# Kernel optimization log

Measured on AMD Instinct MI355X. Metric: run time of the kernel, lower is better.

## Reference

```python
import jax, jax.numpy as jnp
import numpy as np

N, D = 16384, 512
MARGIN = 2.0
EPS = 1e-6  # torch TripletMarginLoss default eps added inside pairwise distance


def setup_inputs() -> dict:
    key = jax.random.key(0)
    k1, k2 = jax.random.split(key)
    inputs = jax.random.normal(k1, (N, D), dtype=jnp.float32)
    positive = jax.random.normal(k2, (N, D), dtype=jnp.float32)
    return {"inputs": inputs, "positive": positive}


def reference(inputs, positive):
    # pairwise squared euclidean distances: ||xi||^2 + ||xj||^2 - 2 xi.xj
    sq = jnp.sum(inputs * inputs, axis=1)                      # [n]
    dist2 = sq[:, None] + sq[None, :] - 2.0 * (inputs @ inputs.T)  # [n,n]
    dist = jnp.sqrt(jnp.clip(dist2, 1e-12))                    # [n,n]
    # original does full argsort per row but only uses index 2 (3rd smallest);
    # top_k on negated distances selects the 3 smallest efficiently.
    _, idx3 = jax.lax.top_k(-dist, 3)                          # [n,3]
    negative = inputs[idx3[:, 2]]                              # [n,d]
    # TripletMarginLoss(margin, p=2): mean(relu(||a-p+eps|| - ||a-n+eps|| + m))
    d_ap = jnp.linalg.norm(inputs - positive + EPS, axis=1)
    d_an = jnp.linalg.norm(inputs - negative + EPS, axis=1)
    loss = jnp.mean(jnp.maximum(d_ap - d_an + MARGIN, 0.0))
    return loss
```

## Files before the change

kernel.cpp:

```cpp
#include <hip/hip_runtime.h>
#include <hip/hip_bf16.h>
#include <hip/hip_fp8.h>
#include <stdint.h>

#define NN 16384
#define DD 512
#define MARGINV 2.0f
#define EPSV 1e-6f

#define BJ 32
#define JGROUPS 8
#define JRANGE (NN / JGROUPS)
#define NTILES (JRANGE / BJ)
#define ROWQ 512
#define TILEB (BJ * ROWQ)
#define SQOFF (2 * TILEB)

#define KEYMASK  0xFFFFC000
#define KEYINITF __builtin_bit_cast(float, 0x7F000000)
#define BIASV 640.0f

typedef __attribute__((ext_vector_type(4))) float f32x4;
typedef __attribute__((ext_vector_type(4))) int   i32x4;
typedef __attribute__((ext_vector_type(8))) int   i32x8;

#define UNIT_SCALE 0x7F

__device__ inline void kins3f(float u, float& m0, float& m1, float& m2) {
  m2 = __builtin_amdgcn_fmed3f(m1, m2, u);
  m1 = __builtin_amdgcn_fmed3f(m0, m1, u);
  m0 = fminf(m0, u);
}

extern "C" __global__ __launch_bounds__(256)
void prep_kernel(const float* __restrict__ x, unsigned char* __restrict__ xq,
                 float* __restrict__ sqb, float* __restrict__ out) {
  if (blockIdx.x == 0 && threadIdx.x == 0) out[0] = 0.0f;
  int row  = blockIdx.x * 4 + (threadIdx.x >> 6);
  int lane = threadIdx.x & 63;
  const float* xr = x + (size_t)row * DD + lane * 8;
  f32x4 a = *(const f32x4*)xr;
  f32x4 b = *(const f32x4*)(xr + 4);
  float s = a[0]*a[0]+a[1]*a[1]+a[2]*a[2]+a[3]*a[3]
          + b[0]*b[0]+b[1]*b[1]+b[2]*b[2]+b[3]*b[3];
  #pragma unroll
  for (int off = 1; off < 64; off <<= 1) s += __shfl_xor(s, off, 64);
  unsigned long long pk = 0;
  #pragma unroll
  for (int t = 0; t < 4; ++t) {
    __hip_fp8_e4m3 qa(a[t]), qb(b[t]);
    pk |= ((unsigned long long)qa.__x) << (8 * t);
    pk |= ((unsigned long long)qb.__x) << (8 * (t + 4));
  }
  *(unsigned long long*)(xq + (size_t)row * ROWQ + lane * 8) = pk;
  if (lane == 0) sqb[row] = s + BIASV;
}

extern "C" __global__ __launch_bounds__(256, 2)
void knn_kernel(const unsigned char* __restrict__ xq, const float* __restrict__ sqb,
                int* __restrict__ pk) {
  __shared__ __align__(16) char lds[2 * TILEB + 8192];
  const int tid  = threadIdx.x;
  const int wave = tid >> 6;
  const int lane = tid & 63;
  const int quad = lane >> 4;
  const int r16  = lane & 15;
  const int bi   = blockIdx.x >> 3;
  const int bj   = blockIdx.x & 7;
  const int ibase = bi * 256 + wave * 64;
  const int jbase = bj * JRANGE;

  #pragma unroll
  for (int p = 0; p < 2; ++p) {
    const float* gs = sqb + jbase + p * 1024 + wave * 256 + lane * 4;
    char* ld = lds + SQOFF + p * 4096 + wave * 1024;
    __builtin_amdgcn_global_load_lds((const __attribute__((address_space(1))) void*)gs,
                                     (__attribute__((address_space(3))) void*)ld,
                                     16, 0, 0);
  }

  i32x8 afr[4][4];
  #pragma unroll
  for (int s = 0; s < 4; ++s) {
    const unsigned char* ar = xq + (size_t)(ibase + s * 16 + r16) * ROWQ + quad * 32;
    #pragma unroll
    for (int c = 0; c < 4; ++c)
      afr[s][c] = *(const i32x8*)(ar + c * 128);
  }

  float m0[16], m1[16], m2[16];
  #pragma unroll
  for (int q = 0; q < 16; ++q) { m0[q] = m1[q] = m2[q] = KEYINITF; }

  auto stage = [&](int jt, int buf) {
    const int jrow0 = jbase + jt * BJ;
    #pragma unroll
    for (int p = 0; p < 4; ++p) {
      const int rr = wave * 8 + p * 2;
      const int lr = rr + (lane >> 5);
      const int u  = (lane & 31) ^ (lr & 7);
      const unsigned char* gsrc = xq + (size_t)(jrow0 + lr) * ROWQ + u * 16;
      char* ldst = lds + buf * TILEB + rr * ROWQ;
      __builtin_amdgcn_global_load_lds((const __attribute__((address_space(1))) void*)gsrc,
                                       (__attribute__((address_space(3))) void*)ldst,
                                       16, 0, 0);
    }
  };

  const int sw = r16 & 7;
  stage(0, 0);
  for (int jt = 0; jt < NTILES; ++jt) {
    __syncthreads();
    if (jt + 1 < NTILES) stage(jt + 1, (jt + 1) & 1);
    #pragma unroll
    for (int jh = 0; jh < 2; ++jh) {
      const char* brow = lds + (jt & 1) * TILEB + (jh * 16 + r16) * ROWQ;
      const float sqj = *(const float*)(lds + SQOFF + ((jt * BJ + jh * 16 + r16) << 2));
      f32x4 acc[4] = {{0.f,0.f,0.f,0.f},{0.f,0.f,0.f,0.f},
                      {0.f,0.f,0.f,0.f},{0.f,0.f,0.f,0.f}};
      #pragma unroll
      for (int c = 0; c < 4; ++c) {
        const int g0 = c * 8 + quad * 2;
        i32x4 lo = *(const i32x4*)(brow + ((g0       ^ sw) * 16));
        i32x4 hi = *(const i32x4*)(brow + (((g0 + 1) ^ sw) * 16));
        i32x8 bf = i32x8{lo[0],lo[1],lo[2],lo[3],hi[0],hi[1],hi[2],hi[3]};
        #pragma unroll
        for (int s = 0; s < 4; ++s)
          acc[s] = __builtin_amdgcn_mfma_scale_f32_16x16x128_f8f6f4(
                     afr[s][c], bf, acc[s], 0, 0, 0, UNIT_SCALE, 0, UNIT_SCALE);
      }
      const int j = jbase + jt * BJ + jh * 16 + r16;
      #pragma unroll
      for (int s = 0; s < 4; ++s) {
        #pragma unroll
        for (int r = 0; r < 4; ++r) {
          float v = fmaf(-2.0f, acc[s][r], sqj);
          int   b = (__builtin_bit_cast(int, v) & KEYMASK) | j;
          kins3f(__builtin_bit_cast(float, b), m0[s*4+r], m1[s*4+r], m2[s*4+r]);
        }
      }
    }
  }

  #pragma unroll
  for (int m = 1; m <= 8; m <<= 1) {
    #pragma unroll
    for (int q = 0; q < 16; ++q) {
      float o0 = __shfl_xor(m0[q], m, 64);
      float o1 = __shfl_xor(m1[q], m, 64);
      float o2 = __shfl_xor(m2[q], m, 64);
      kins3f(o0, m0[q], m1[q], m2[q]);
      kins3f(o1, m0[q], m1[q], m2[q]);
      kins3f(o2, m0[q], m1[q], m2[q]);
    }
  }

  #pragma unroll
  for (int q = 0; q < 16; ++q) {
    if (r16 == q) {
      int s  = q >> 2, r = q & 3;
      int gi = ibase + s * 16 + quad * 4 + r;
      int ob = (gi * JGROUPS + bj) * 3;
      pk[ob + 0] = __builtin_bit_cast(int, m0[q]);
      pk[ob + 1] = __builtin_bit_cast(int, m1[q]);
      pk[ob + 2] = __builtin_bit_cast(int, m2[q]);
    }
  }
}

extern "C" __global__ __launch_bounds__(256)
void finalize_kernel(const float* __restrict__ x, const float* __restrict__ pos,
                     const int* __restrict__ pk, float* __restrict__ out) {
  __shared__ float wsum[4];
  int wave = threadIdx.x >> 6;
  int lane = threadIdx.x & 63;
  float acc = 0.f;
  #pragma unroll
  for (int rep = 0; rep < 8; ++rep) {
    int i = rep * 2048 + blockIdx.x * 4 + wave;
    int neg = 0;
    if (lane == 0) {
      float m0 = KEYINITF, m1 = KEYINITF, m2 = KEYINITF;
      #pragma unroll
      for (int s = 0; s < JGROUPS * 3; ++s) {
        kins3f(__builtin_bit_cast(float, pk[i * (JGROUPS * 3) + s]), m0, m1, m2);
      }
      neg = __builtin_bit_cast(int, m2) & 0x3FFF;
    }
    neg = __shfl(neg, 0, 64);
    const float* xr = x   + (size_t)i * DD + lane * 8;
    const float* pr = pos + (size_t)i * DD + lane * 8;
    const float* nr = x   + (size_t)neg * DD + lane * 8;
    f32x4 xa = *(const f32x4*)xr, xb4 = *(const f32x4*)(xr + 4);
    f32x4 pa = *(const f32x4*)pr, pb  = *(const f32x4*)(pr + 4);
    f32x4 na = *(const f32x4*)nr, nb  = *(const f32x4*)(nr + 4);
    float sap = 0.f, san = 0.f;
    #pragma unroll
    for (int k = 0; k < 4; ++k) {
      float d0 = xa[k]  - pa[k] + EPSV; sap = fmaf(d0, d0, sap);
      float d1 = xa[k]  - na[k] + EPSV; san = fmaf(d1, d1, san);
      float d2 = xb4[k] - pb[k] + EPSV; sap = fmaf(d2, d2, sap);
      float d3 = xb4[k] - nb[k] + EPSV; san = fmaf(d3, d3, san);
    }
    #pragma unroll
    for (int off = 1; off < 64; off <<= 1) {
      sap += __shfl_xor(sap, off, 64);
      san += __shfl_xor(san, off, 64);
    }
    if (lane == 0) {
      float l = sqrtf(sap) - sqrtf(san) + MARGINV;
      acc += (l > 0.f ? l : 0.f);
    }
  }
  if (lane == 0) wsum[wave] = acc;
  __syncthreads();
  if (threadIdx.x == 0) {
    atomicAdd(out, (wsum[0] + wsum[1] + wsum[2] + wsum[3]) * (1.0f / NN));
  }
}

extern "C" void kernel_launch(void* const* d_in, const int* in_sizes, int n_in,
                              void* d_out, int out_size, void* d_ws, size_t ws_size,
                              hipStream_t stream) {
  const float* x   = (const float*)d_in[0];
  const float* pos = (const float*)d_in[1];
  char* ws = (char*)d_ws;
  unsigned char* xq  = (unsigned char*)ws;
  float* sqb = (float*)(ws + (size_t)NN * ROWQ);
  int*   pk  = (int*)  (ws + (size_t)NN * ROWQ + (size_t)NN * 4);

  prep_kernel<<<NN / 4, 256, 0, stream>>>(x, xq, sqb, (float*)d_out);
  knn_kernel<<<(NN / 256) * JGROUPS, 256, 0, stream>>>(xq, sqb, pk);
  finalize_kernel<<<512, 256, 0, stream>>>(x, pos, pk, (float*)d_out);
}
```

Before: 237.0 us.

## Overlap kNN epilogue with next MFMA block and track top-2 excluding self

Restructures the kNN inner loop into a software pipeline with two alternating accumulator sets, so the key/min-insertion epilogue of one 16-column half runs interleaved with the MFMAs of the next, and raises wave priority around MFMA issue. It also drops the third-smallest tracking by masking the self-distance on diagonal tiles and keeping only the top-2, which shrinks registers, insertion work and the partial-result buffer. The fp8 packing in prep uses the packed hardware convert intrinsic. The risk is that assuming self is always the minimum could differ from the reference under fp8 quantization ties, and the macro pipeline raises register pressure.

After: 468.2 us. +97.5%, slower.

```diff
diff --git a/kernel.cpp b/kernel.cpp
--- a/kernel.cpp
+++ b/kernel.cpp
@@ -18,6 +18,7 @@
 
 #define KEYMASK  0xFFFFC000
 #define KEYINITF __builtin_bit_cast(float, 0x7F000000)
+#define PSINIT   __builtin_bit_cast(float, 0x7F7C0000)
 #define BIASV 640.0f
 
 typedef __attribute__((ext_vector_type(4))) float f32x4;
@@ -25,12 +26,6 @@
 typedef __attribute__((ext_vector_type(8))) int   i32x8;
 
 #define UNIT_SCALE 0x7F
-
-__device__ inline void kins3f(float u, float& m0, float& m1, float& m2) {
-  m2 = __builtin_amdgcn_fmed3f(m1, m2, u);
-  m1 = __builtin_amdgcn_fmed3f(m0, m1, u);
-  m0 = fminf(m0, u);
-}
 
 extern "C" __global__ __launch_bounds__(256)
 void prep_kernel(const float* __restrict__ x, unsigned char* __restrict__ xq,
@@ -45,14 +40,12 @@
           + b[0]*b[0]+b[1]*b[1]+b[2]*b[2]+b[3]*b[3];
   #pragma unroll
   for (int off = 1; off < 64; off <<= 1) s += __shfl_xor(s, off, 64);
-  unsigned long long pk = 0;
-  #pragma unroll
-  for (int t = 0; t < 4; ++t) {
-    __hip_fp8_e4m3 qa(a[t]), qb(b[t]);
-    pk |= ((unsigned long long)qa.__x) << (8 * t);
-    pk |= ((unsigned long long)qb.__x) << (8 * (t + 4));
-  }
-  *(unsigned long long*)(xq + (size_t)row * ROWQ + lane * 8) = pk;
+  unsigned int w0 = (unsigned int)__builtin_amdgcn_cvt_pk_fp8_f32(a[0], a[1], 0, false);
+  w0 = (unsigned int)__builtin_amdgcn_cvt_pk_fp8_f32(a[2], a[3], (int)w0, true);
+  unsigned int w1 = (unsigned int)__builtin_amdgcn_cvt_pk_fp8_f32(b[0], b[1], 0, false);
+  w1 = (unsigned int)__builtin_amdgcn_cvt_pk_fp8_f32(b[2], b[3], (int)w1, true);
+  unsigned long long pk8 = ((unsigned long long)w1 << 32) | (unsigned long long)w0;
+  *(unsigned long long*)(xq + (size_t)row * ROWQ + lane * 8) = pk8;
   if (lane == 0) sqb[row] = s + BIASV;
 }
 
@@ -88,9 +81,9 @@
       afr[s][c] = *(const i32x8*)(ar + c * 128);
   }
 
-  float m0[16], m1[16], m2[16];
-  #pragma unroll
-  for (int q = 0; q < 16; ++q) { m0[q] = m1[q] = m2[q] = KEYINITF; }
+  float m0[16], m1[16];
+  #pragma unroll
+  for (int q = 0; q < 16; ++q) { m0[q] = m1[q] = KEYINITF; }
 
   auto stage = [&](int jt, int buf) {
     const int jrow0 = jbase + jt * BJ;
@@ -108,39 +101,79 @@
   };
 
   const int sw = r16 & 7;
+
+  f32x4 accA[4], accB[4];
+  #pragma unroll
+  for (int s = 0; s < 4; ++s) { accA[s] = f32x4{0.f,0.f,0.f,0.f}; accB[s] = f32x4{0.f,0.f,0.f,0.f}; }
+  float psqj  = PSINIT;
+  int   pj    = 0;
+  bool  pdiag = false;
+
+#define EPI(A) do {                                                              \
+    if (pdiag) {                                                                 \
+      _Pragma("unroll") for (int s_ = 0; s_ < 4; ++s_)                           \
+      _Pragma("unroll") for (int r_ = 0; r_ < 4; ++r_) {                         \
+        float v_ = fmaf(-2.0f, A[s_][r_], psqj);                                 \
+        int   b_ = (__builtin_bit_cast(int, v_) & KEYMASK) | pj;                 \
+        float u_ = __builtin_bit_cast(float, b_);                                \
+        u_ = (pj == (ibase + s_ * 16 + quad * 4 + r_)) ? KEYINITF : u_;          \
+        m1[s_*4+r_] = __builtin_amdgcn_fmed3f(m0[s_*4+r_], m1[s_*4+r_], u_);     \
+        m0[s_*4+r_] = fminf(m0[s_*4+r_], u_);                                    \
+      }                                                                          \
+    } else {                                                                     \
+      _Pragma("unroll") for (int s_ = 0; s_ < 4; ++s_)                           \
+      _Pragma("unroll") for (int r_ = 0; r_ < 4; ++r_) {                         \
+        float v_ = fmaf(-2.0f, A[s_][r_], psqj);                                 \
+        int   b_ = (__builtin_bit_cast(int, v_) & KEYMASK) | pj;                 \
+        float u_ = __builtin_bit_cast(float, b_);                                \
+        m1[s_*4+r_] = __builtin_amdgcn_fmed3f(m0[s_*4+r_], m1[s_*4+r_], u_);     \
+        m0[s_*4+r_] = fminf(m0[s_*4+r_], u_);                                    \
+      }                                                                          \
+    }                                                                            \
+  } while (0)
+
+#define LDC(BLO, BHI, CC) do {                                                   \
+    const int g0_ = (CC) * 8 + quad * 2;                                         \
+    BLO = *(const i32x4*)(brow + ((g0_ ^ sw) * 16));                             \
+    BHI = *(const i32x4*)(brow + (((g0_ + 1) ^ sw) * 16));                       \
+  } while (0)
+
+#define MF4(BLO, BHI, CC, ACC) do {                                              \
+    i32x8 bf_ = i32x8{BLO[0],BLO[1],BLO[2],BLO[3],BHI[0],BHI[1],BHI[2],BHI[3]};  \
+    __builtin_amdgcn_s_setprio(1);                                               \
+    _Pragma("unroll") for (int s_ = 0; s_ < 4; ++s_)                             \
+      ACC[s_] = __builtin_amdgcn_mfma_scale_f32_16x16x128_f8f6f4(                \
+                  afr[s_][(CC)], bf_, ACC[s_], 0, 0, 0, UNIT_SCALE, 0, UNIT_SCALE); \
+    __builtin_amdgcn_s_setprio(0);                                               \
+  } while (0)
+
+#define JHBODY(JT, JH, ACCW, ACCR, DIAGT) do {                                   \
+    const char* brow = lds + ((JT) & 1) * TILEB + ((JH) * 16 + r16) * ROWQ;      \
+    const float sqj_ = *(const float*)(lds + SQOFF + (((JT) * BJ + (JH) * 16 + r16) << 2)); \
+    const int j_ = jbase + (JT) * BJ + (JH) * 16 + r16;                          \
+    i32x4 b0lo, b0hi, b1lo, b1hi;                                                \
+    LDC(b0lo, b0hi, 0);                                                          \
+    LDC(b1lo, b1hi, 1);                                                          \
+    _Pragma("unroll") for (int s_ = 0; s_ < 4; ++s_) ACCW[s_] = f32x4{0.f,0.f,0.f,0.f}; \
+    MF4(b0lo, b0hi, 0, ACCW);                                                    \
+    LDC(b0lo, b0hi, 2);                                                          \
+    MF4(b1lo, b1hi, 1, ACCW);                                                    \
+    LDC(b1lo, b1hi, 3);                                                          \
+    EPI(ACCR);                \
+    MF4(b0lo, b0hi, 2, ACCW);                                                    \
+    MF4(b1lo, b1hi, 3, ACCW);                                                    \
+    psqj = sqj_; pj = j_; pdiag = (DIAGT);                                       \
+  } while (0)
+
   stage(0, 0);
   for (int jt = 0; jt < NTILES; ++jt) {
     __syncthreads();
     if (jt + 1 < NTILES) stage(jt + 1, (jt + 1) & 1);
-    #pragma unroll
-    for (int jh = 0; jh < 2; ++jh) {
-      const char* brow = lds + (jt & 1) * TILEB + (jh * 16 + r16) * ROWQ;
-      const float sqj = *(const float*)(lds + SQOFF + ((jt * BJ + jh * 16 + r16) << 2));
-      f32x4 acc[4] = {{0.f,0.f,0.f,0.f},{0.f,0.f,0.f,0.f},
-                      {0.f,0.f,0.f,0.f},{0.f,0.f,0.f,0.f}};
-      #pragma unroll
-      for (int c = 0; c < 4; ++c) {
-        const int g0 = c * 8 + quad * 2;
-        i32x4 lo = *(const i32x4*)(brow + ((g0       ^ sw) * 16));
-        i32x4 hi = *(const i32x4*)(brow + (((g0 + 1) ^ sw) * 16));
-        i32x8 bf = i32x8{lo[0],lo[1],lo[2],lo[3],hi[0],hi[1],hi[2],hi[3]};
-        #pragma unroll
-        for (int s = 0; s < 4; ++s)
-          acc[s] = __builtin_amdgcn_mfma_scale_f32_16x16x128_f8f6f4(
-                     afr[s][c], bf, acc[s], 0, 0, 0, UNIT_SCALE, 0, UNIT_SCALE);
-      }
-      const int j = jbase + jt * BJ + jh * 16 + r16;
-      #pragma unroll
-      for (int s = 0; s < 4; ++s) {
-        #pragma unroll
-        for (int r = 0; r < 4; ++r) {
-          float v = fmaf(-2.0f, acc[s][r], sqj);
-          int   b = (__builtin_bit_cast(int, v) & KEYMASK) | j;
-          kins3f(__builtin_bit_cast(float, b), m0[s*4+r], m1[s*4+r], m2[s*4+r]);
-        }
-      }
-    }
-  }
+    const bool diagt = ((bi >> 3) == bj) && ((jt >> 3) == (bi & 7));
+    JHBODY(jt, 0, accA, accB, diagt);
+    JHBODY(jt, 1, accB, accA, diagt);
+  }
+  EPI(accB);
 
   #pragma unroll
   for (int m = 1; m <= 8; m <<= 1) {
@@ -148,10 +181,10 @@
     for (int q = 0; q < 16; ++q) {
       float o0 = __shfl_xor(m0[q], m, 64);
       float o1 = __shfl_xor(m1[q], m, 64);
-      float o2 = __shfl_xor(m2[q], m, 64);
-      kins3f(o0, m0[q], m1[q], m2[q]);
-      kins3f(o1, m0[q], m1[q], m2[q]);
-      kins3f(o2, m0[q], m1[q], m2[q]);
+      m1[q] = __builtin_amdgcn_fmed3f(m0[q], m1[q], o0);
+      m0[q] = fminf(m0[q], o0);
+      m1[q] = __builtin_amdgcn_fmed3f(m0[q], m1[q], o1);
+      m0[q] = fminf(m0[q], o1);
     }
   }
 
@@ -160,12 +193,15 @@
     if (r16 == q) {
       int s  = q >> 2, r = q & 3;
       int gi = ibase + s * 16 + quad * 4 + r;
-      int ob = (gi * JGROUPS + bj) * 3;
+      int ob = (gi * JGROUPS + bj) * 2;
       pk[ob + 0] = __builtin_bit_cast(int, m0[q]);
       pk[ob + 1] = __builtin_bit_cast(int, m1[q]);
-      pk[ob + 2] = __builtin_bit_cast(int, m2[q]);
-    }
-  }
+    }
+  }
+#undef EPI
+#undef LDC
+#undef MF4
+#undef JHBODY
 }
 
 extern "C" __global__ __launch_bounds__(256)
@@ -180,12 +216,14 @@
     int i = rep * 2048 + blockIdx.x * 4 + wave;
     int neg = 0;
     if (lane == 0) {
-      float m0 = KEYINITF, m1 = KEYINITF, m2 = KEYINITF;
+      float m0 = KEYINITF, m1 = KEYINITF;
       #pragma unroll
-      for (int s = 0; s < JGROUPS * 3; ++s) {
-        kins3f(__builtin_bit_cast(float, pk[i * (JGROUPS * 3) + s]), m0, m1, m2);
+      for (int s = 0; s < JGROUPS * 2; ++s) {
+        float u = __builtin_bit_cast(float, pk[i * (JGROUPS * 2) + s]);
+        m1 = __builtin_amdgcn_fmed3f(m0, m1, u);
+        m0 = fminf(m0, u);
       }
-      neg = __builtin_bit_cast(int, m2) & 0x3FFF;
+      neg = __builtin_bit_cast(int, m1) & 0x3FFF;
     }
     neg = __shfl(neg, 0, 64);
     const float* xr = x   + (size_t)i * DD + lane * 8;
```
